# Kernel tuning notes

Measured on AMD Instinct MI355X. Metric: run time of the kernel, lower is better.

Reference implementation:

```python
import math
import jax, jax.numpy as jnp
import numpy as np

VOCAB, D_MODEL, N_HEADS, D_FF, N_LAYERS = 32000, 1024, 16, 4096, 6
B, S = 4, 1024
D_K = D_MODEL // N_HEADS
EPS = 1e-5


def make_pe(max_len, d_model):
    pos = np.arange(max_len, dtype=np.float32)[:, None]
    div = np.exp(np.arange(0, d_model, 2, dtype=np.float32) * (-math.log(10000.0) / d_model))
    pe = np.zeros((max_len, d_model), dtype=np.float32)
    pe[:, 0::2] = np.sin(pos * div)
    pe[:, 1::2] = np.cos(pos * div)
    return jnp.asarray(pe)


def setup_inputs() -> dict:
    key = jax.random.key(0)
    ks = jax.random.split(key, 20)
    sd = 0.02
    L = N_LAYERS
    return {
        "src": jax.random.randint(ks[0], (B, S), 0, VOCAB),
        "src_mask": jnp.ones((B, 1, 1, S), dtype=jnp.int32),
        "emb": jax.random.normal(ks[1], (VOCAB, D_MODEL), jnp.float32) * sd,
        "pe": make_pe(5000, D_MODEL),
        # attention projections, stored [in, out] so y = x @ W + b
        "wq": jax.random.normal(ks[2], (L, D_MODEL, D_MODEL), jnp.float32) * sd,
        "bq": jnp.zeros((L, D_MODEL), jnp.float32),
        "wk": jax.random.normal(ks[3], (L, D_MODEL, D_MODEL), jnp.float32) * sd,
        "bk": jnp.zeros((L, D_MODEL), jnp.float32),
        "wv": jax.random.normal(ks[4], (L, D_MODEL, D_MODEL), jnp.float32) * sd,
        "bv": jnp.zeros((L, D_MODEL), jnp.float32),
        "wo": jax.random.normal(ks[5], (L, D_MODEL, D_MODEL), jnp.float32) * sd,
        "bo": jnp.zeros((L, D_MODEL), jnp.float32),
        "w1": jax.random.normal(ks[6], (L, D_MODEL, D_FF), jnp.float32) * sd,
        "b1": jnp.zeros((L, D_FF), jnp.float32),
        "w2": jax.random.normal(ks[7], (L, D_FF, D_MODEL), jnp.float32) * sd,
        "b2": jnp.zeros((L, D_MODEL), jnp.float32),
        "g1": jnp.ones((L, D_MODEL), jnp.float32),
        "be1": jnp.zeros((L, D_MODEL), jnp.float32),
        "g2": jnp.ones((L, D_MODEL), jnp.float32),
        "be2": jnp.zeros((L, D_MODEL), jnp.float32),
    }


def layer_norm(x, g, b):
    mu = jnp.mean(x, axis=-1, keepdims=True)
    var = jnp.mean(jnp.square(x - mu), axis=-1, keepdims=True)
    return (x - mu) * jax.lax.rsqrt(var + EPS) * g + b


def mha(x, mask, wq, bq, wk, bk, wv, bv, wo, bo):
    b, s, _ = x.shape
    def split(h):  # [B,S,D] -> [B,H,S,Dk]
        return h.reshape(b, s, N_HEADS, D_K).transpose(0, 2, 1, 3)
    Q = split(x @ wq + bq)
    K = split(x @ wk + bk)
    V = split(x @ wv + bv)
    scores = jnp.einsum("bhqd,bhkd->bhqk", Q, K) * (D_K ** -0.5)
    scores = jnp.where(mask == 0, jnp.float32(-1e9), scores)
    attn = jax.nn.softmax(scores, axis=-1)
    out = jnp.einsum("bhqk,bhkd->bhqd", attn, V)
    out = out.transpose(0, 2, 1, 3).reshape(b, s, D_MODEL)
    return out @ wo + bo


def encoder(src, src_mask, emb, pe, wq, bq, wk, bk, wv, bv, wo, bo,
            w1, b1, w2, b2, g1, be1, g2, be2):
    x = emb[src] * math.sqrt(D_MODEL) + pe[: src.shape[1]][None]
    for l in range(N_LAYERS):
        a = mha(x, src_mask, wq[l], bq[l], wk[l], bk[l], wv[l], bv[l], wo[l], bo[l])
        x = layer_norm(x + a, g1[l], be1[l])
        f = jax.nn.relu(x @ w1[l] + b1[l]) @ w2[l] + b2[l]
        x = layer_norm(x + f, g2[l], be2[l])
    return x


def reference(src, src_mask, emb, pe, wq, bq, wk, bk, wv, bv, wo, bo,
              w1, b1, w2, b2, g1, be1, g2, be2):
    return encoder(src, src_mask, emb, pe, wq, bq, wk, bk, wv, bv, wo, bo,
                   w1, b1, w2, b2, g1, be1, g2, be2)
```

## Files before the change

### kernel.cpp

```cpp
#include <hip/hip_runtime.h>
#include <stdint.h>
#include <stddef.h>

typedef unsigned short u16;
typedef u16   u16x8 __attribute__((ext_vector_type(8)));
typedef __bf16 bf16x8 __attribute__((ext_vector_type(8)));
typedef float f32x4 __attribute__((ext_vector_type(4)));

#define DM   1024
#define NTOK 4096
#define DFF  4096
#define LN_EPS 1e-5f

__device__ __forceinline__ u16 f2b(float f) {
  union { float f; unsigned u; } v; v.f = f;
  unsigned r = (v.u + 0x7fffu + ((v.u >> 16) & 1u)) >> 16;
  return (u16)r;
}
__device__ __forceinline__ float b2f(u16 h) {
  union { unsigned u; float f; } v; v.u = ((unsigned)h) << 16;
  return v.f;
}
__device__ __forceinline__ bf16x8 ldfrag(const u16* p) {
  u16x8 v = *(const u16x8*)p;
  return __builtin_bit_cast(bf16x8, v);
}

__global__ __launch_bounds__(256) void embed_kernel(
    const int* __restrict__ src, const float* __restrict__ emb,
    const float* __restrict__ pe, float* __restrict__ x, u16* __restrict__ xb) {
  int tk = blockIdx.x;
  int s  = tk & 1023;
  int id = src[tk];
  int d  = threadIdx.x * 4;
  float4 e = *(const float4*)(emb + (size_t)id * DM + d);
  float4 p = *(const float4*)(pe + (size_t)s * DM + d);
  float4 v;
  v.x = e.x * 32.0f + p.x; v.y = e.y * 32.0f + p.y;
  v.z = e.z * 32.0f + p.z; v.w = e.w * 32.0f + p.w;
  size_t base = (size_t)tk * DM + d;
  *(float4*)(x + base) = v;
  xb[base + 0] = f2b(v.x); xb[base + 1] = f2b(v.y);
  xb[base + 2] = f2b(v.z); xb[base + 3] = f2b(v.w);
}

__global__ __launch_bounds__(256) void convt_kernel(
    const float* __restrict__ s0, const float* __restrict__ s1,
    const float* __restrict__ s2, const float* __restrict__ s3,
    u16* __restrict__ d0, u16* __restrict__ d1, u16* __restrict__ d2, u16* __restrict__ d3,
    int K, int N) {
  int z = blockIdx.z;
  const float* src = (z == 0) ? s0 : (z == 1) ? s1 : (z == 2) ? s2 : s3;
  u16* dst = (z == 0) ? d0 : (z == 1) ? d1 : (z == 2) ? d2 : d3;
  __shared__ float tile[32][33];
  int n0 = blockIdx.x * 32, k0 = blockIdx.y * 32;
  int c = threadIdx.x & 31, rq = threadIdx.x >> 5;
#pragma unroll
  for (int i = 0; i < 4; i++) {
    int r = rq + i * 8;
    tile[r][c] = src[(size_t)(k0 + r) * N + n0 + c];
  }
  __syncthreads();
#pragma unroll
  for (int i = 0; i < 4; i++) {
    int r = rq + i * 8;
    dst[(size_t)(n0 + r) * K + k0 + c] = f2b(tile[c][r]);
  }
}

template <int MODE>
__global__ __launch_bounds__(256) void gemm_kernel(
    const u16* __restrict__ A,
    const u16* __restrict__ Bt0, const u16* __restrict__ Bt1, const u16* __restrict__ Bt2,
    const float* __restrict__ bias0, const float* __restrict__ bias1, const float* __restrict__ bias2,
    void* out0, void* out1, void* out2,
    int M, int N, int K) {
  int z = blockIdx.z;
  const u16* Bt = (z == 0) ? Bt0 : (z == 1) ? Bt1 : Bt2;
  const float* bias = (z == 0) ? bias0 : (z == 1) ? bias1 : bias2;
  void* outv = (z == 0) ? out0 : (z == 1) ? out1 : out2;

  __shared__ u16 As[128 * 32];
  __shared__ u16 Bs[128 * 32];

  const int t = threadIdx.x;
  const int lane = t & 63;
  const int w = t >> 6;
  const int g = lane >> 4;
  const int r = lane & 15;
  const int m0 = blockIdx.y * 128;
  const int n0 = blockIdx.x * 128;
  const int mh = (w & 1) * 64;
  const int nh = (w >> 1) * 64;

  f32x4 acc[4][4];
#pragma unroll
  for (int i = 0; i < 4; i++)
#pragma unroll
    for (int j = 0; j < 4; j++) acc[i][j] = (f32x4){0.f, 0.f, 0.f, 0.f};

  const int srow = t >> 2;
  const int scol = (t & 3) * 8;

  for (int k0 = 0; k0 < K; k0 += 32) {
#pragma unroll
    for (int p = 0; p < 2; p++) {
      int row = p * 64 + srow;
      u16x8 av = *(const u16x8*)(A + (size_t)(m0 + row) * K + k0 + scol);
      *(u16x8*)&As[p * 2048 + t * 8] = av;
      u16x8 bv = *(const u16x8*)(Bt + (size_t)(n0 + row) * K + k0 + scol);
      *(u16x8*)&Bs[p * 2048 + t * 8] = bv;
    }
    __syncthreads();

    bf16x8 af[4], bfm[4];
#pragma unroll
    for (int mt = 0; mt < 4; mt++) af[mt] = ldfrag(&As[(mh + mt * 16 + r) * 32 + g * 8]);
#pragma unroll
    for (int nt = 0; nt < 4; nt++) bfm[nt] = ldfrag(&Bs[(nh + nt * 16 + r) * 32 + g * 8]);
#pragma unroll
    for (int mt = 0; mt < 4; mt++)
#pragma unroll
      for (int nt = 0; nt < 4; nt++)
        acc[mt][nt] = __builtin_amdgcn_mfma_f32_16x16x32_bf16(af[mt], bfm[nt], acc[mt][nt], 0, 0, 0);
    __syncthreads();
  }

#pragma unroll
  for (int mt = 0; mt < 4; mt++) {
#pragma unroll
    for (int nt = 0; nt < 4; nt++) {
      int col = n0 + nh + nt * 16 + r;
      float bv = bias[col];
#pragma unroll
      for (int rr = 0; rr < 4; rr++) {
        int row = m0 + mh + mt * 16 + g * 4 + rr;
        float v = acc[mt][nt][rr] + bv;
        if (MODE == 2) v = fmaxf(v, 0.0f);
        if (MODE == 0)
          ((float*)outv)[(size_t)row * N + col] = v;
        else
          ((u16*)outv)[(size_t)row * N + col] = f2b(v);
      }
    }
  }
}

__global__ __launch_bounds__(256) void attn_kernel(
    const u16* __restrict__ qb, const u16* __restrict__ kb,
    const u16* __restrict__ vb, u16* __restrict__ ob) {
  __shared__ u16 Qs[64 * 64];
  __shared__ u16 Ks[64 * 64];
  __shared__ u16 Vs[64 * 64];
  __shared__ u16 Ps[4][16 * 64];

  const int t = threadIdx.x;
  const int lane = t & 63;
  const int w = t >> 6;
  const int g = lane >> 4;
  const int r = lane & 15;
  const int q0 = blockIdx.x * 64;
  const int h = blockIdx.y;
  const int b = blockIdx.z;
  const size_t hoff = (size_t)h * 64;

#pragma unroll
  for (int p = 0; p < 2; p++) {
    int row = p * 32 + (t >> 3);
    int col = (t & 7) * 8;
    *(u16x8*)&Qs[row * 64 + col] =
        *(const u16x8*)(qb + ((size_t)(b * 1024 + q0 + row)) * DM + hoff + col);
  }

  f32x4 acc[4];
#pragma unroll
  for (int dt = 0; dt < 4; dt++) acc[dt] = (f32x4){0.f, 0.f, 0.f, 0.f};
  float m_r[4] = {-1e30f, -1e30f, -1e30f, -1e30f};
  float l_r[4] = {0.f, 0.f, 0.f, 0.f};

  for (int kc = 0; kc < 16; kc++) {
    int key0 = kc * 64;
    __syncthreads();
#pragma unroll
    for (int p = 0; p < 2; p++) {
      int row = p * 32 + (t >> 3);
      int col = (t & 7) * 8;
      *(u16x8*)&Ks[row * 64 + col] =
          *(const u16x8*)(kb + ((size_t)(b * 1024 + key0 + row)) * DM + hoff + col);
    }
#pragma unroll
    for (int p = 0; p < 2; p++) {
      int key = p * 32 + (t >> 3);
      int dg = t & 7;
      u16x8 vv = *(const u16x8*)(vb + ((size_t)(b * 1024 + key0 + key)) * DM + hoff + dg * 8);
#pragma unroll
      for (int j = 0; j < 8; j++) Vs[(dg * 8 + j) * 64 + key] = vv[j];
    }
    __syncthreads();

    f32x4 sf[4];
#pragma unroll
    for (int kt = 0; kt < 4; kt++) sf[kt] = (f32x4){0.f, 0.f, 0.f, 0.f};
#pragma unroll
    for (int ks = 0; ks < 2; ks++) {
      bf16x8 aq = ldfrag(&Qs[(w * 16 + r) * 64 + ks * 32 + g * 8]);
#pragma unroll
      for (int kt = 0; kt < 4; kt++) {
        bf16x8 bk = ldfrag(&Ks[(kt * 16 + r) * 64 + ks * 32 + g * 8]);
        sf[kt] = __builtin_amdgcn_mfma_f32_16x16x32_bf16(aq, bk, sf[kt], 0, 0, 0);
      }
    }

    float mx[4] = {-1e30f, -1e30f, -1e30f, -1e30f};
#pragma unroll
    for (int kt = 0; kt < 4; kt++)
#pragma unroll
      for (int rr = 0; rr < 4; rr++) mx[rr] = fmaxf(mx[rr], sf[kt][rr] * 0.125f);
#pragma unroll
    for (int off = 1; off < 16; off <<= 1)
#pragma unroll
      for (int rr = 0; rr < 4; rr++) mx[rr] = fmaxf(mx[rr], __shfl_xor(mx[rr], off));

    float mnew[4], alpha[4], sum[4];
#pragma unroll
    for (int rr = 0; rr < 4; rr++) {
      mnew[rr] = fmaxf(m_r[rr], mx[rr]);
      alpha[rr] = __expf(m_r[rr] - mnew[rr]);
      sum[rr] = 0.f;
    }
#pragma unroll
    for (int kt = 0; kt < 4; kt++)
#pragma unroll
      for (int rr = 0; rr < 4; rr++) {
        float p = __expf(sf[kt][rr] * 0.125f - mnew[rr]);
        sum[rr] += p;
        Ps[w][(g * 4 + rr) * 64 + kt * 16 + r] = f2b(p);
      }
#pragma unroll
    for (int off = 1; off < 16; off <<= 1)
#pragma unroll
      for (int rr = 0; rr < 4; rr++) sum[rr] += __shfl_xor(sum[rr], off);
#pragma unroll
    for (int rr = 0; rr < 4; rr++) {
      l_r[rr] = l_r[rr] * alpha[rr] + sum[rr];
      m_r[rr] = mnew[rr];
    }
#pragma unroll
    for (int dt = 0; dt < 4; dt++)
#pragma unroll
      for (int rr = 0; rr < 4; rr++) acc[dt][rr] *= alpha[rr];

    __syncthreads();

#pragma unroll
    for (int ks = 0; ks < 2; ks++) {
      bf16x8 ap = ldfrag(&Ps[w][r * 64 + ks * 32 + g * 8]);
#pragma unroll
      for (int dt = 0; dt < 4; dt++) {
        bf16x8 bv = ldfrag(&Vs[(dt * 16 + r) * 64 + ks * 32 + g * 8]);
        acc[dt] = __builtin_amdgcn_mfma_f32_16x16x32_bf16(ap, bv, acc[dt], 0, 0, 0);
      }
    }
  }

#pragma unroll
  for (int dt = 0; dt < 4; dt++)
#pragma unroll
    for (int rr = 0; rr < 4; rr++) {
      int qrow = q0 + w * 16 + g * 4 + rr;
      float val = acc[dt][rr] / l_r[rr];
      ob[((size_t)(b * 1024 + qrow)) * DM + hoff + dt * 16 + r] = f2b(val);
    }
}

__device__ __forceinline__ float block_sum256(float v, float* red) {
  int lane = threadIdx.x & 63, w = threadIdx.x >> 6;
#pragma unroll
  for (int off = 32; off > 0; off >>= 1) v += __shfl_down(v, off);
  if (lane == 0) red[w] = v;
  __syncthreads();
  float s = red[0] + red[1] + red[2] + red[3];
  __syncthreads();
  return s;
}

__global__ __launch_bounds__(256) void add_ln_kernel(
    const float* __restrict__ xin, const float* __restrict__ tres,
    const float* __restrict__ gain, const float* __restrict__ beta,
    float* __restrict__ xout, u16* __restrict__ xbout) {
  __shared__ float red[4];
  int row = blockIdx.x, t = threadIdx.x;
  size_t base = (size_t)row * DM;
  float v[4];
  float s = 0.f;
#pragma unroll
  for (int i = 0; i < 4; i++) {
    int d = t + i * 256;
    v[i] = xin[base + d] + tres[base + d];
    s += v[i];
  }
  float total = block_sum256(s, red);
  float mu = total * (1.0f / 1024.0f);
  float q = 0.f;
#pragma unroll
  for (int i = 0; i < 4; i++) {
    float dd = v[i] - mu;
    q += dd * dd;
  }
  float total2 = block_sum256(q, red);
  float rstd = rsqrtf(total2 * (1.0f / 1024.0f) + LN_EPS);
#pragma unroll
  for (int i = 0; i < 4; i++) {
    int d = t + i * 256;
    float y = (v[i] - mu) * rstd * gain[d] + beta[d];
    xout[base + d] = y;
    xbout[base + d] = f2b(y);
  }
}

extern "C" void kernel_launch(void* const* d_in, const int* in_sizes, int n_in,
                              void* d_out, int out_size, void* d_ws, size_t ws_size,
                              hipStream_t stream) {
  const int* src  = (const int*)d_in[0];
  const float* emb = (const float*)d_in[2];
  const float* pe  = (const float*)d_in[3];
  const float* wq = (const float*)d_in[4];  const float* bq = (const float*)d_in[5];
  const float* wk = (const float*)d_in[6];  const float* bk = (const float*)d_in[7];
  const float* wv = (const float*)d_in[8];  const float* bv = (const float*)d_in[9];
  const float* wo = (const float*)d_in[10]; const float* bo = (const float*)d_in[11];
  const float* w1 = (const float*)d_in[12]; const float* b1 = (const float*)d_in[13];
  const float* w2 = (const float*)d_in[14]; const float* b2 = (const float*)d_in[15];
  const float* g1 = (const float*)d_in[16]; const float* be1 = (const float*)d_in[17];
  const float* g2 = (const float*)d_in[18]; const float* be2 = (const float*)d_in[19];
  float* out = (float*)d_out;

  char* p = (char*)d_ws;
  auto take = [&](size_t bytes) {
    char* q = p;
    p += (bytes + 255) & ~(size_t)255;
    return (void*)q;
  };
  u16* wqt = (u16*)take((size_t)DM * DM * 2);
  u16* wkt = (u16*)take((size_t)DM * DM * 2);
  u16* wvt = (u16*)take((size_t)DM * DM * 2);
  u16* wot = (u16*)take((size_t)DM * DM * 2);
  u16* w1t = (u16*)take((size_t)DFF * DM * 2);
  u16* w2t = (u16*)take((size_t)DM * DFF * 2);
  float* x  = (float*)take((size_t)NTOK * DM * 4);
  u16* xb   = (u16*)take((size_t)NTOK * DM * 2);
  u16* qbuf = (u16*)take((size_t)NTOK * DM * 2);
  u16* kbuf = (u16*)take((size_t)NTOK * DM * 2);
  u16* vbuf = (u16*)take((size_t)NTOK * DM * 2);
  u16* obuf = (u16*)take((size_t)NTOK * DM * 2);
  float* tb = (float*)take((size_t)NTOK * DM * 4);
  u16* hb   = (u16*)take((size_t)NTOK * DFF * 2);

  embed_kernel<<<NTOK, 256, 0, stream>>>(src, emb, pe, x, xb);

  for (int l = 0; l < 6; l++) {
    const float* wql = wq + (size_t)l * DM * DM;
    const float* wkl = wk + (size_t)l * DM * DM;
    const float* wvl = wv + (size_t)l * DM * DM;
    const float* wol = wo + (size_t)l * DM * DM;
    const float* w1l = w1 + (size_t)l * DM * DFF;
    const float* w2l = w2 + (size_t)l * DFF * DM;

    convt_kernel<<<dim3(32, 32, 4), 256, 0, stream>>>(wql, wkl, wvl, wol,
                                                      wqt, wkt, wvt, wot, DM, DM);
    convt_kernel<<<dim3(128, 32, 1), 256, 0, stream>>>(w1l, w1l, w1l, w1l,
                                                       w1t, w1t, w1t, w1t, DM, DFF);
    convt_kernel<<<dim3(32, 128, 1), 256, 0, stream>>>(w2l, w2l, w2l, w2l,
                                                       w2t, w2t, w2t, w2t, DFF, DM);

    gemm_kernel<1><<<dim3(8, 32, 3), 256, 0, stream>>>(
        xb, wqt, wkt, wvt, bq + (size_t)l * DM, bk + (size_t)l * DM, bv + (size_t)l * DM,
        qbuf, kbuf, vbuf, NTOK, DM, DM);

    attn_kernel<<<dim3(16, 16, 4), 256, 0, stream>>>(qbuf, kbuf, vbuf, obuf);

    gemm_kernel<0><<<dim3(8, 32, 1), 256, 0, stream>>>(
        obuf, wot, wot, wot, bo + (size_t)l * DM, bo + (size_t)l * DM, bo + (size_t)l * DM,
        tb, tb, tb, NTOK, DM, DM);

    add_ln_kernel<<<NTOK, 256, 0, stream>>>(x, tb, g1 + (size_t)l * DM, be1 + (size_t)l * DM, x, xb);

    gemm_kernel<2><<<dim3(32, 32, 1), 256, 0, stream>>>(
        xb, w1t, w1t, w1t, b1 + (size_t)l * DFF, b1 + (size_t)l * DFF, b1 + (size_t)l * DFF,
        hb, hb, hb, NTOK, DFF, DM);

    gemm_kernel<0><<<dim3(8, 32, 1), 256, 0, stream>>>(
        hb, w2t, w2t, w2t, b2 + (size_t)l * DM, b2 + (size_t)l * DM, b2 + (size_t)l * DM,
        tb, tb, tb, NTOK, DM, DFF);

    float* xo = (l == 5) ? out : x;
    add_ln_kernel<<<NTOK, 256, 0, stream>>>(x, tb, g2 + (size_t)l * DM, be2 + (size_t)l * DM, xo, xb);
  }
}
```

Measured before the change: 2.432 ms.

## Use direct global-to-LDS loads in GEMM, restructure attention, vectorize elementwise kernels

The GEMM now stages A and B tiles with global_load_lds instead of register round-trips, and gains an M-tile template parameter so the N=1024 output GEMMs use 64-row tiles and launch twice as many blocks. Attention is rewritten: a separate kernel pre-transposes V, each wave handles 32 queries with Q held in registers, K and V fragments are read straight from global memory, there is no block-level synchronisation, and the softmax uses exp2 with a folded scale. The embed and add+layernorm kernels switch to vector loads and stores. These changes target staging overhead, barrier stalls and low occupancy, at the cost of an extra transpose pass and more scattered global reads in attention.

```diff
diff --git a/kernel.cpp b/kernel.cpp
--- a/kernel.cpp
+++ b/kernel.cpp
@@ -3,6 +3,8 @@
 #include <stddef.h>
 
 typedef unsigned short u16;
+typedef u16   u16x2 __attribute__((ext_vector_type(2)));
+typedef u16   u16x4 __attribute__((ext_vector_type(4)));
 typedef u16   u16x8 __attribute__((ext_vector_type(8)));
 typedef __bf16 bf16x8 __attribute__((ext_vector_type(8)));
 typedef float f32x4 __attribute__((ext_vector_type(4)));
@@ -12,18 +14,21 @@
 #define DFF  4096
 #define LN_EPS 1e-5f
 
+#define EXP2F(x) __builtin_amdgcn_exp2f(x)
+
 __device__ __forceinline__ u16 f2b(float f) {
   union { float f; unsigned u; } v; v.f = f;
   unsigned r = (v.u + 0x7fffu + ((v.u >> 16) & 1u)) >> 16;
   return (u16)r;
 }
-__device__ __forceinline__ float b2f(u16 h) {
-  union { unsigned u; float f; } v; v.u = ((unsigned)h) << 16;
-  return v.f;
-}
 __device__ __forceinline__ bf16x8 ldfrag(const u16* p) {
   u16x8 v = *(const u16x8*)p;
   return __builtin_bit_cast(bf16x8, v);
+}
+__device__ __forceinline__ void gl2lds16(const void* g, void* l) {
+  __builtin_amdgcn_global_load_lds(
+      (const __attribute__((address_space(1))) uint32_t*)g,
+      (__attribute__((address_space(3))) uint32_t*)l, 16, 0, 0);
 }
 
 __global__ __launch_bounds__(256) void embed_kernel(
@@ -40,8 +45,8 @@
   v.z = e.z * 32.0f + p.z; v.w = e.w * 32.0f + p.w;
   size_t base = (size_t)tk * DM + d;
   *(float4*)(x + base) = v;
-  xb[base + 0] = f2b(v.x); xb[base + 1] = f2b(v.y);
-  xb[base + 2] = f2b(v.z); xb[base + 3] = f2b(v.w);
+  u16x4 pk = { f2b(v.x), f2b(v.y), f2b(v.z), f2b(v.w) };
+  *(u16x4*)(xb + base) = pk;
 }
 
 __global__ __launch_bounds__(256) void convt_kernel(
@@ -68,7 +73,27 @@
   }
 }
 
-template <int MODE>
+__global__ __launch_bounds__(256) void vtrans_kernel(
+    const u16* __restrict__ vbuf, u16* __restrict__ vt) {
+  __shared__ u16 Ts[64 * 72];
+  int t = threadIdx.x;
+  int stile = blockIdx.x;
+  int h = blockIdx.y, b = blockIdx.z;
+  int s = t >> 2, c = (t & 3) * 16;
+  const u16* src = vbuf + ((size_t)(b * 1024 + stile * 64 + s)) * DM + h * 64 + c;
+  *(u16x8*)&Ts[s * 72 + c]     = *(const u16x8*)src;
+  *(u16x8*)&Ts[s * 72 + c + 8] = *(const u16x8*)(src + 8);
+  __syncthreads();
+  int d = t >> 2, s0 = (t & 3) * 16;
+  u16 tmp[16];
+#pragma unroll
+  for (int i = 0; i < 16; i++) tmp[i] = Ts[(s0 + i) * 72 + d];
+  u16* dst = vt + ((size_t)((b * 16 + h) * 64 + d)) * 1024 + stile * 64 + s0;
+  *(u16x8*)dst       = *(u16x8*)&tmp[0];
+  *(u16x8*)(dst + 8) = *(u16x8*)&tmp[8];
+}
+
+template <int MODE, int MT>
 __global__ __launch_bounds__(256) void gemm_kernel(
     const u16* __restrict__ A,
     const u16* __restrict__ Bt0, const u16* __restrict__ Bt1, const u16* __restrict__ Bt2,
@@ -80,7 +105,7 @@
   const float* bias = (z == 0) ? bias0 : (z == 1) ? bias1 : bias2;
   void* outv = (z == 0) ? out0 : (z == 1) ? out1 : out2;
 
-  __shared__ u16 As[128 * 32];
+  __shared__ u16 As[MT * 32];
   __shared__ u16 Bs[128 * 32];
 
   const int t = threadIdx.x;
@@ -88,54 +113,57 @@
   const int w = t >> 6;
   const int g = lane >> 4;
   const int r = lane & 15;
-  const int m0 = blockIdx.y * 128;
+  const int m0 = blockIdx.y * MT;
   const int n0 = blockIdx.x * 128;
-  const int mh = (w & 1) * 64;
+  const int mh = (w & 1) * (MT / 2);
   const int nh = (w >> 1) * 64;
-
-  f32x4 acc[4][4];
-#pragma unroll
-  for (int i = 0; i < 4; i++)
+  constexpr int MI = MT / 32;
+
+  f32x4 acc[MI][4];
+#pragma unroll
+  for (int i = 0; i < MI; i++)
 #pragma unroll
     for (int j = 0; j < 4; j++) acc[i][j] = (f32x4){0.f, 0.f, 0.f, 0.f};
 
-  const int srow = t >> 2;
-  const int scol = (t & 3) * 8;
+  const int lrow = lane >> 2;
+  const int lcol = (lane & 3) * 8;
 
   for (int k0 = 0; k0 < K; k0 += 32) {
 #pragma unroll
+    for (int p = 0; p < MT / 64; p++) {
+      int rbase = w * (MT / 4) + p * 16;
+      gl2lds16(A + (size_t)(m0 + rbase + lrow) * K + k0 + lcol, &As[rbase * 32]);
+    }
+#pragma unroll
     for (int p = 0; p < 2; p++) {
-      int row = p * 64 + srow;
-      u16x8 av = *(const u16x8*)(A + (size_t)(m0 + row) * K + k0 + scol);
-      *(u16x8*)&As[p * 2048 + t * 8] = av;
-      u16x8 bv = *(const u16x8*)(Bt + (size_t)(n0 + row) * K + k0 + scol);
-      *(u16x8*)&Bs[p * 2048 + t * 8] = bv;
+      int rbase = w * 32 + p * 16;
+      gl2lds16(Bt + (size_t)(n0 + rbase + lrow) * K + k0 + lcol, &Bs[rbase * 32]);
     }
     __syncthreads();
 
-    bf16x8 af[4], bfm[4];
-#pragma unroll
-    for (int mt = 0; mt < 4; mt++) af[mt] = ldfrag(&As[(mh + mt * 16 + r) * 32 + g * 8]);
+    bf16x8 af[MI], bfm[4];
+#pragma unroll
+    for (int mi = 0; mi < MI; mi++) af[mi] = ldfrag(&As[(mh + mi * 16 + r) * 32 + g * 8]);
 #pragma unroll
     for (int nt = 0; nt < 4; nt++) bfm[nt] = ldfrag(&Bs[(nh + nt * 16 + r) * 32 + g * 8]);
 #pragma unroll
-    for (int mt = 0; mt < 4; mt++)
+    for (int mi = 0; mi < MI; mi++)
 #pragma unroll
       for (int nt = 0; nt < 4; nt++)
-        acc[mt][nt] = __builtin_amdgcn_mfma_f32_16x16x32_bf16(af[mt], bfm[nt], acc[mt][nt], 0, 0, 0);
+        acc[mi][nt] = __builtin_amdgcn_mfma_f32_16x16x32_bf16(af[mi], bfm[nt], acc[mi][nt], 0, 0, 0);
     __syncthreads();
   }
 
 #pragma unroll
-  for (int mt = 0; mt < 4; mt++) {
+  for (int mi = 0; mi < MI; mi++) {
 #pragma unroll
     for (int nt = 0; nt < 4; nt++) {
       int col = n0 + nh + nt * 16 + r;
       float bv = bias[col];
 #pragma unroll
       for (int rr = 0; rr < 4; rr++) {
-        int row = m0 + mh + mt * 16 + g * 4 + rr;
-        float v = acc[mt][nt][rr] + bv;
+        int row = m0 + mh + mi * 16 + g * 4 + rr;
+        float v = acc[mi][nt][rr] + bv;
         if (MODE == 2) v = fmaxf(v, 0.0f);
         if (MODE == 0)
           ((float*)outv)[(size_t)row * N + col] = v;
@@ -148,129 +176,122 @@
 
 __global__ __launch_bounds__(256) void attn_kernel(
     const u16* __restrict__ qb, const u16* __restrict__ kb,
-    const u16* __restrict__ vb, u16* __restrict__ ob) {
-  __shared__ u16 Qs[64 * 64];
-  __shared__ u16 Ks[64 * 64];
-  __shared__ u16 Vs[64 * 64];
-  __shared__ u16 Ps[4][16 * 64];
+    const u16* __restrict__ vt, u16* __restrict__ ob) {
+  __shared__ u16 Ps[4][32 * 72];
 
   const int t = threadIdx.x;
   const int lane = t & 63;
   const int w = t >> 6;
   const int g = lane >> 4;
   const int r = lane & 15;
-  const int q0 = blockIdx.x * 64;
+  const int qbase = blockIdx.x * 128 + w * 32;
   const int h = blockIdx.y;
   const int b = blockIdx.z;
   const size_t hoff = (size_t)h * 64;
-
-#pragma unroll
-  for (int p = 0; p < 2; p++) {
-    int row = p * 32 + (t >> 3);
-    int col = (t & 7) * 8;
-    *(u16x8*)&Qs[row * 64 + col] =
-        *(const u16x8*)(qb + ((size_t)(b * 1024 + q0 + row)) * DM + hoff + col);
-  }
-
-  f32x4 acc[4];
-#pragma unroll
-  for (int dt = 0; dt < 4; dt++) acc[dt] = (f32x4){0.f, 0.f, 0.f, 0.f};
-  float m_r[4] = {-1e30f, -1e30f, -1e30f, -1e30f};
-  float l_r[4] = {0.f, 0.f, 0.f, 0.f};
+  const u16* vth = vt + ((size_t)(b * 16 + h) * 64) * 1024;
+
+  const float SC2 = 0.125f * 1.44269504088896f;
+
+  bf16x8 qf[2][2];
+#pragma unroll
+  for (int nt = 0; nt < 2; nt++)
+#pragma unroll
+    for (int ks = 0; ks < 2; ks++)
+      qf[nt][ks] = ldfrag(qb + ((size_t)(b * 1024 + qbase + nt * 16 + r)) * DM + hoff + ks * 32 + g * 8);
+
+  f32x4 o_acc[2][4];
+#pragma unroll
+  for (int nt = 0; nt < 2; nt++)
+#pragma unroll
+    for (int dt = 0; dt < 4; dt++) o_acc[nt][dt] = (f32x4){0.f, 0.f, 0.f, 0.f};
+  float m_r[2] = {-1e30f, -1e30f};
+  float l_r[2] = {0.f, 0.f};
 
   for (int kc = 0; kc < 16; kc++) {
-    int key0 = kc * 64;
-    __syncthreads();
-#pragma unroll
-    for (int p = 0; p < 2; p++) {
-      int row = p * 32 + (t >> 3);
-      int col = (t & 7) * 8;
-      *(u16x8*)&Ks[row * 64 + col] =
-          *(const u16x8*)(kb + ((size_t)(b * 1024 + key0 + row)) * DM + hoff + col);
-    }
-#pragma unroll
-    for (int p = 0; p < 2; p++) {
-      int key = p * 32 + (t >> 3);
-      int dg = t & 7;
-      u16x8 vv = *(const u16x8*)(vb + ((size_t)(b * 1024 + key0 + key)) * DM + hoff + dg * 8);
-#pragma unroll
-      for (int j = 0; j < 8; j++) Vs[(dg * 8 + j) * 64 + key] = vv[j];
-    }
-    __syncthreads();
-
-    f32x4 sf[4];
-#pragma unroll
-    for (int kt = 0; kt < 4; kt++) sf[kt] = (f32x4){0.f, 0.f, 0.f, 0.f};
+    const int key0 = kc * 64;
+
+    f32x4 st[2][4];
+#pragma unroll
+    for (int nt = 0; nt < 2; nt++)
+#pragma unroll
+      for (int kt = 0; kt < 4; kt++) st[nt][kt] = (f32x4){0.f, 0.f, 0.f, 0.f};
 #pragma unroll
     for (int ks = 0; ks < 2; ks++) {
-      bf16x8 aq = ldfrag(&Qs[(w * 16 + r) * 64 + ks * 32 + g * 8]);
+      bf16x8 kf[4];
+#pragma unroll
+      for (int kt = 0; kt < 4; kt++)
+        kf[kt] = ldfrag(kb + ((size_t)(b * 1024 + key0 + kt * 16 + r)) * DM + hoff + ks * 32 + g * 8);
+#pragma unroll
+      for (int nt = 0; nt < 2; nt++)
+#pragma unroll
+        for (int kt = 0; kt < 4; kt++)
+          st[nt][kt] = __builtin_amdgcn_mfma_f32_16x16x32_bf16(kf[kt], qf[nt][ks], st[nt][kt], 0, 0, 0);
+    }
+
+#pragma unroll
+    for (int nt = 0; nt < 2; nt++) {
+      float mx = -1e30f;
+#pragma unroll
+      for (int kt = 0; kt < 4; kt++)
+#pragma unroll
+        for (int rr = 0; rr < 4; rr++) mx = fmaxf(mx, st[nt][kt][rr]);
+      mx *= SC2;
+      mx = fmaxf(mx, __shfl_xor(mx, 16));
+      mx = fmaxf(mx, __shfl_xor(mx, 32));
+      float mnew = fmaxf(m_r[nt], mx);
+      float alpha = EXP2F(m_r[nt] - mnew);
+      m_r[nt] = mnew;
+      float sum = 0.f;
 #pragma unroll
       for (int kt = 0; kt < 4; kt++) {
-        bf16x8 bk = ldfrag(&Ks[(kt * 16 + r) * 64 + ks * 32 + g * 8]);
-        sf[kt] = __builtin_amdgcn_mfma_f32_16x16x32_bf16(aq, bk, sf[kt], 0, 0, 0);
+        u16x4 pk;
+#pragma unroll
+        for (int rr = 0; rr < 4; rr++) {
+          float p = EXP2F(st[nt][kt][rr] * SC2 - mnew);
+          sum += p;
+          pk[rr] = f2b(p);
+        }
+        *(u16x4*)&Ps[w][(nt * 16 + r) * 72 + kt * 16 + g * 4] = pk;
       }
-    }
-
-    float mx[4] = {-1e30f, -1e30f, -1e30f, -1e30f};
-#pragma unroll
-    for (int kt = 0; kt < 4; kt++)
-#pragma unroll
-      for (int rr = 0; rr < 4; rr++) mx[rr] = fmaxf(mx[rr], sf[kt][rr] * 0.125f);
-#pragma unroll
-    for (int off = 1; off < 16; off <<= 1)
-#pragma unroll
-      for (int rr = 0; rr < 4; rr++) mx[rr] = fmaxf(mx[rr], __shfl_xor(mx[rr], off));
-
-    float mnew[4], alpha[4], sum[4];
+      sum += __shfl_xor(sum, 16);
+      sum += __shfl_xor(sum, 32);
+      l_r[nt] = l_r[nt] * alpha + sum;
+#pragma unroll
+      for (int rr = 0; rr < 4; rr++) {
+        float arow = __shfl(alpha, g * 4 + rr);
+#pragma unroll
+        for (int dt = 0; dt < 4; dt++) o_acc[nt][dt][rr] *= arow;
+      }
+    }
+
+#pragma unroll
+    for (int ks = 0; ks < 2; ks++) {
+      bf16x8 pf[2];
+#pragma unroll
+      for (int nt = 0; nt < 2; nt++)
+        pf[nt] = ldfrag(&Ps[w][(nt * 16 + r) * 72 + ks * 32 + g * 8]);
+#pragma unroll
+      for (int dt = 0; dt < 4; dt++) {
+        bf16x8 vf = ldfrag(vth + ((size_t)(dt * 16 + r)) * 1024 + key0 + ks * 32 + g * 8);
+#pragma unroll
+        for (int nt = 0; nt < 2; nt++)
+          o_acc[nt][dt] = __builtin_amdgcn_mfma_f32_16x16x32_bf16(pf[nt], vf, o_acc[nt][dt], 0, 0, 0);
+      }
+    }
+  }
+
+#pragma unroll
+  for (int nt = 0; nt < 2; nt++) {
 #pragma unroll
     for (int rr = 0; rr < 4; rr++) {
-      mnew[rr] = fmaxf(m_r[rr], mx[rr]);
-      alpha[rr] = __expf(m_r[rr] - mnew[rr]);
-      sum[rr] = 0.f;
-    }
-#pragma unroll
-    for (int kt = 0; kt < 4; kt++)
-#pragma unroll
-      for (int rr = 0; rr < 4; rr++) {
-        float p = __expf(sf[kt][rr] * 0.125f - mnew[rr]);
-        sum[rr] += p;
-        Ps[w][(g * 4 + rr) * 64 + kt * 16 + r] = f2b(p);
+      float linv = 1.0f / __shfl(l_r[nt], g * 4 + rr);
+      int q = qbase + nt * 16 + g * 4 + rr;
+#pragma unroll
+      for (int dt = 0; dt < 4; dt++) {
+        ob[((size_t)(b * 1024 + q)) * DM + hoff + dt * 16 + r] = f2b(o_acc[nt][dt][rr] * linv);
       }
-#pragma unroll
-    for (int off = 1; off < 16; off <<= 1)
-#pragma unroll
-      for (int rr = 0; rr < 4; rr++) sum[rr] += __shfl_xor(sum[rr], off);
-#pragma unroll
-    for (int rr = 0; rr < 4; rr++) {
-      l_r[rr] = l_r[rr] * alpha[rr] + sum[rr];
-      m_r[rr] = mnew[rr];
-    }
-#pragma unroll
-    for (int dt = 0; dt < 4; dt++)
-#pragma unroll
-      for (int rr = 0; rr < 4; rr++) acc[dt][rr] *= alpha[rr];
-
-    __syncthreads();
-
-#pragma unroll
-    for (int ks = 0; ks < 2; ks++) {
-      bf16x8 ap = ldfrag(&Ps[w][r * 64 + ks * 32 + g * 8]);
-#pragma unroll
-      for (int dt = 0; dt < 4; dt++) {
-        bf16x8 bv = ldfrag(&Vs[(dt * 16 + r) * 64 + ks * 32 + g * 8]);
-        acc[dt] = __builtin_amdgcn_mfma_f32_16x16x32_bf16(ap, bv, acc[dt], 0, 0, 0);
-      }
-    }
-  }
-
-#pragma unroll
-  for (int dt = 0; dt < 4; dt++)
-#pragma unroll
-    for (int rr = 0; rr < 4; rr++) {
-      int qrow = q0 + w * 16 + g * 4 + rr;
-      float val = acc[dt][rr] / l_r[rr];
-      ob[((size_t)(b * 1024 + qrow)) * DM + hoff + dt * 16 + r] = f2b(val);
-    }
+    }
+  }
 }
 
 __device__ __forceinline__ float block_sum256(float v, float* red) {
@@ -291,31 +312,27 @@
   __shared__ float red[4];
   int row = blockIdx.x, t = threadIdx.x;
   size_t base = (size_t)row * DM;
-  float v[4];
-  float s = 0.f;
-#pragma unroll
-  for (int i = 0; i < 4; i++) {
-    int d = t + i * 256;
-    v[i] = xin[base + d] + tres[base + d];
-    s += v[i];
-  }
-  float total = block_sum256(s, red);
+  int d = t * 4;
+  float4 a = *(const float4*)(xin + base + d);
+  float4 bb = *(const float4*)(tres + base + d);
+  float4 v;
+  v.x = a.x + bb.x; v.y = a.y + bb.y; v.z = a.z + bb.z; v.w = a.w + bb.w;
+  float total = block_sum256(v.x + v.y + v.z + v.w, red);
   float mu = total * (1.0f / 1024.0f);
-  float q = 0.f;
-#pragma unroll
-  for (int i = 0; i < 4; i++) {
-    float dd = v[i] - mu;
-    q += dd * dd;
-  }
-  float total2 = block_sum256(q, red);
+  float qx = (v.x - mu) * (v.x - mu) + (v.y - mu) * (v.y - mu) +
+             (v.z - mu) * (v.z - mu) + (v.w - mu) * (v.w - mu);
+  float total2 = block_sum256(qx, red);
   float rstd = rsqrtf(total2 * (1.0f / 1024.0f) + LN_EPS);
-#pragma unroll
-  for (int i = 0; i < 4; i++) {
-    int d = t + i * 256;
-    float y = (v[i] - mu) * rstd * gain[d] + beta[d];
-    xout[base + d] = y;
-    xbout[base + d] = f2b(y);
-  }
+  float4 gg = *(const float4*)(gain + d);
+  float4 be = *(const float4*)(beta + d);
+  float4 y;
+  y.x = (v.x - mu) * rstd * gg.x + be.x;
+  y.y = (v.y - mu) * rstd * gg.y + be.y;
+  y.z = (v.z - mu) * rstd * gg.z + be.z;
+  y.w = (v.w - mu) * rstd * gg.w + be.w;
+  *(float4*)(xout + base + d) = y;
+  u16x4 pk = { f2b(y.x), f2b(y.y), f2b(y.z), f2b(y.w) };
+  *(u16x4*)(xbout + base + d) = pk;
 }
 
 extern "C" void kernel_launch(void* const* d_in, const int* in_sizes, int n_in,
@@ -351,6 +368,7 @@
   u16* qbuf = (u16*)take((size_t)NTOK * DM * 2);
   u16* kbuf = (u16*)take((size_t)NTOK * DM * 2);
   u16* vbuf = (u16*)take((size_t)NTOK * DM * 2);
+  u16* vtb  = (u16*)take((size_t)NTOK * DM * 2);
   u16* obuf = (u16*)take((size_t)NTOK * DM * 2);
   float* tb = (float*)take((size_t)NTOK * DM * 4);
   u16* hb   = (u16*)take((size_t)NTOK * DFF * 2);
@@ -372,23 +390,25 @@
     convt_kernel<<<dim3(32, 128, 1), 256, 0, stream>>>(w2l, w2l, w2l, w2l,
                                                        w2t, w2t, w2t, w2t, DFF, DM);
 
-    gemm_kernel<1><<<dim3(8, 32, 3), 256, 0, stream>>>(
+    gemm_kernel<1, 128><<<dim3(8, 32, 3), 256, 0, stream>>>(
         xb, wqt, wkt, wvt, bq + (size_t)l * DM, bk + (size_t)l * DM, bv + (size_t)l * DM,
         qbuf, kbuf, vbuf, NTOK, DM, DM);
 
-    attn_kernel<<<dim3(16, 16, 4), 256, 0, stream>>>(qbuf, kbuf, vbuf, obuf);
-
-    gemm_kernel<0><<<dim3(8, 32, 1), 256, 0, stream>>>(
+    vtrans_kernel<<<dim3(16, 16, 4), 256, 0, stream>>>(vbuf, vtb);
+
+    attn_kernel<<<dim3(8, 16, 4), 256, 0, stream>>>(qbuf, kbuf, vtb, obuf);
+
+    gemm_kernel<0, 64><<<dim3(8, 64, 1), 256, 0, stream>>>(
         obuf, wot, wot, wot, bo + (size_t)l * DM, bo + (size_t)l * DM, bo + (size_t)l * DM,
         tb, tb, tb, NTOK, DM, DM);
 
     add_ln_kernel<<<NTOK, 256, 0, stream>>>(x, tb, g1 + (size_t)l * DM, be1 + (size_t)l * DM, x, xb);
 
-    gemm_kernel<2><<<dim3(32, 32, 1), 256, 0, stream>>>(
+    gemm_kernel<2, 128><<<dim3(32, 32, 1), 256, 0, stream>>>(
         xb, w1t, w1t, w1t, b1 + (size_t)l * DFF, b1 + (size_t)l * DFF, b1 + (size_t)l * DFF,
         hb, hb, hb, NTOK, DFF, DM);
 
-    gemm_kernel<0><<<dim3(8, 32, 1), 256, 0, stream>>>(
+    gemm_kernel<0, 64><<<dim3(8, 64, 1), 256, 0, stream>>>(
         hb, w2t, w2t, w2t, b2 + (size_t)l * DM, b2 + (size_t)l * DM, b2 + (size_t)l * DM,
         tb, tb, tb, NTOK, DM, DFF);
 
```

Measured after the change: 2.125 ms. -12.6%, faster.
